# Performance work log

Measured on AMD Instinct MI355X. Metric: run time of the kernel, lower is better.

## Reference

```python
import jax, jax.numpy as jnp
import numpy as np

E, T, N = 120000, 800000, 12000
H, INT, BE, R, S, NB = 128, 64, 8, 6, 7, 2
SR = S * R  # 42 = num_spherical * num_radial
OE, OC = 256, 1
CUTOFF = 5.0
P_ENV = 6  # envelope_exponent + 1


def _glorot(k, shape):
    fan = shape[-2] + shape[-1]
    return jax.random.normal(k, shape, jnp.float32) * jnp.sqrt(2.0 / fan)


def setup_inputs() -> dict:
    key = jax.random.key(0)
    ki = iter(jax.random.split(key, 40))
    inp = {}
    inp["x"] = jax.random.normal(next(ki), (E, H), jnp.float32)
    # distances in (0.5, 4.9) so envelope 1/d term is well behaved
    inp["dist"] = 0.5 + 4.4 * jax.random.uniform(next(ki), (E,), jnp.float32)
    inp["freq"] = jnp.arange(1, R + 1, dtype=jnp.float32) * jnp.pi  # BesselBasisLayer init
    inp["sbf"] = jax.random.normal(next(ki), (T, SR), jnp.float32)
    inp["idx_kj"] = jax.random.randint(next(ki), (T,), 0, E)
    inp["idx_ji"] = jax.random.randint(next(ki), (T,), 0, E)
    inp["edge_i"] = jax.random.randint(next(ki), (E,), 0, N)
    inp["num_nodes"] = N
    inp["Wi_rbf1"] = _glorot(next(ki), (NB, R, BE))
    inp["Wi_rbf2"] = _glorot(next(ki), (NB, BE, H))
    inp["Wi_sbf1"] = _glorot(next(ki), (NB, SR, BE))
    inp["Wi_sbf2"] = _glorot(next(ki), (NB, BE, INT))
    inp["Wi_kj"] = _glorot(next(ki), (NB, H, H))
    inp["bi_kj"] = jnp.zeros((NB, H), jnp.float32)
    inp["Wi_ji"] = _glorot(next(ki), (NB, H, H))
    inp["bi_ji"] = jnp.zeros((NB, H), jnp.float32)
    inp["Wi_down"] = _glorot(next(ki), (NB, H, INT))
    inp["Wi_up"] = _glorot(next(ki), (NB, INT, H))
    inp["Wi_res"] = _glorot(next(ki), (NB, 3, 2, H, H))  # 1 before-skip + 2 after-skip residuals
    inp["bi_res"] = jnp.zeros((NB, 3, 2, H), jnp.float32)
    inp["Wi_lin"] = _glorot(next(ki), (NB, H, H))
    inp["bi_lin"] = jnp.zeros((NB, H), jnp.float32)
    inp["Wo_rbf"] = _glorot(next(ki), (NB + 1, R, H))
    inp["Wo_up"] = _glorot(next(ki), (NB + 1, H, OE))
    inp["bo_up"] = jnp.zeros((NB + 1, OE), jnp.float32)
    inp["Wo_lin"] = _glorot(next(ki), (NB + 1, 3, OE, OE))
    inp["bo_lin"] = jnp.zeros((NB + 1, 3, OE), jnp.float32)
    inp["Wo_out"] = _glorot(next(ki), (NB + 1, OE, OC))
    return inp


def reference(x, dist, freq, sbf,
              Wi_rbf1, Wi_rbf2, Wi_sbf1, Wi_sbf2, Wi_kj, bi_kj, Wi_ji, bi_ji,
              Wi_down, Wi_up, Wi_res, bi_res, Wi_lin, bi_lin,
              Wo_rbf, Wo_up, bo_up, Wo_lin, bo_lin, Wo_out,
              idx_kj, idx_ji, edge_i, num_nodes):
    act = jax.nn.silu  # swish
    num_edges = x.shape[0]

    # BesselBasisLayer with Envelope(p=6): a=-28, b=48, c=-21
    d = dist / CUTOFF                       # [E]
    d5 = d ** (P_ENV - 1)
    env = 1.0 / d - 28.0 * d5 + 48.0 * d5 * d - 21.0 * d5 * d * d
    rbf = env[:, None] * jnp.sin(freq[None, :] * d[:, None])  # [E, R]

    def output_block(b, xe):
        g = (rbf @ Wo_rbf[b]) * xe                                   # [E, H]
        nodes = jax.ops.segment_sum(g, edge_i, num_segments=num_nodes)  # [N, H]
        h = nodes @ Wo_up[b] + bo_up[b]
        for l in range(Wo_lin.shape[1]):
            h = act(h @ Wo_lin[b, l] + bo_lin[b, l])
        return h @ Wo_out[b]                                          # [N, OC]

    def residual(b, r, h):
        t = act(h @ Wi_res[b, r, 0] + bi_res[b, r, 0])
        return h + act(t @ Wi_res[b, r, 1] + bi_res[b, r, 1])

    def interaction(b, xe):
        x_ji = act(xe @ Wi_ji[b] + bi_ji[b])                          # [E, H]
        x_kj = act(xe @ Wi_kj[b] + bi_kj[b])                          # [E, H]
        rb = (rbf @ Wi_rbf1[b]) @ Wi_rbf2[b]                          # [E, H]
        x_kj = act((x_kj * rb) @ Wi_down[b])                          # [E, INT]
        sb = (sbf @ Wi_sbf1[b]) @ Wi_sbf2[b]                          # [T, INT]
        m = x_kj[idx_kj] * sb                                         # gather over triplets
        agg = jax.ops.segment_sum(m, idx_ji, num_segments=num_edges)  # scatter back to edges
        x_kj = act(agg @ Wi_up[b])                                    # [E, H]
        h = x_ji + x_kj
        h = residual(b, 0, h)                                         # before skip
        h = act(h @ Wi_lin[b] + bi_lin[b]) + xe                       # skip
        h = residual(b, 1, h)                                         # after skip
        h = residual(b, 2, h)
        return h

    P = output_block(0, x)
    xe = x
    for b in range(NB):
        xe = interaction(b, xe)
        P = P + output_block(b + 1, xe)
    return P  # [num_nodes, out_channels]
```

## Files before the change

### kernel.cpp

```cpp
#include <hip/hip_runtime.h>
#include <hip/hip_bf16.h>

namespace {
constexpr int E     = 120000;
constexpr int T     = 800000;
constexpr int NN    = 12000;
constexpr int H     = 128;
constexpr int INTD  = 64;
constexpr int BE    = 8;
constexpr int R     = 6;
constexpr int SR    = 42;
constexpr int OE    = 256;
constexpr float CUTOFF = 5.0f;
constexpr int PKB   = 163840;
constexpr int TAILO = 40960;
}

typedef __attribute__((ext_vector_type(8))) short bf16x8;
typedef __attribute__((ext_vector_type(4))) float f32x4;

__device__ __forceinline__ float silu_f(float x) { return x / (1.0f + __expf(-x)); }
__device__ __forceinline__ float4 silu4(float4 v) {
    return make_float4(silu_f(v.x), silu_f(v.y), silu_f(v.z), silu_f(v.w));
}

__device__ __forceinline__ unsigned fbits(float x) {
    union { float f; unsigned u; } v; v.f = x; return v.u;
}
__device__ __forceinline__ float fof(unsigned u) {
    union { float f; unsigned u; } v; v.u = u; return v.f;
}
__device__ __forceinline__ unsigned short bf16_rn(float x) {
    unsigned u = fbits(x);
    unsigned r = u + 0x7FFFu + ((u >> 16) & 1u);
    return (unsigned short)(r >> 16);
}
__device__ __forceinline__ float bf16_f(unsigned short h) { return fof(((unsigned)h) << 16); }

__device__ __forceinline__ void pack2(float x0, float x1, unsigned& h, unsigned& l) {
    const unsigned u0 = fbits(x0), u1 = fbits(x1);
    const unsigned t0 = u0 & 0xFFFF0000u, t1 = u1 & 0xFFFF0000u;
    h = (u0 >> 16) | t1;
    l = (fbits(x0 - fof(t0)) >> 16) | (fbits(x1 - fof(t1)) & 0xFFFF0000u);
}

__global__ void k_rbf(const float* __restrict__ dist, const float* __restrict__ freq,
                      float* __restrict__ rbf) {
    int e = blockIdx.x * blockDim.x + threadIdx.x;
    if (e >= E) return;
    float d  = dist[e] * (1.0f / CUTOFF);
    float d2 = d * d;
    float d5 = d2 * d2 * d;
    float env = 1.0f / d - 28.0f * d5 + 48.0f * d5 * d - 21.0f * d5 * d2;
    #pragma unroll
    for (int i = 0; i < R; ++i) rbf[e * R + i] = env * sinf(freq[i] * d);
}

__global__ void k_count(const int* __restrict__ idx, int n, int* __restrict__ cnt) {
    int i = blockIdx.x * 256 + threadIdx.x;
    if (i < n) atomicAdd(&cnt[idx[i]], 1);
}

__global__ __launch_bounds__(256) void k_red(const int* __restrict__ cnt, int n,
                                             int* __restrict__ bsum) {
    __shared__ int ws[4];
    const int tid = threadIdx.x;
    const int base = blockIdx.x * 2048 + tid * 8;
    int s = 0;
    #pragma unroll
    for (int k = 0; k < 8; ++k) { int i = base + k; s += (i < n) ? cnt[i] : 0; }
    #pragma unroll
    for (int off = 32; off; off >>= 1) s += __shfl_down(s, off);
    if ((tid & 63) == 0) ws[tid >> 6] = s;
    __syncthreads();
    if (tid == 0) bsum[blockIdx.x] = ws[0] + ws[1] + ws[2] + ws[3];
}

__global__ void k_scanb(int* __restrict__ b, int nb) {
    __shared__ int s[64];
    const int tid = threadIdx.x;
    if (tid < nb) s[tid] = b[tid];
    __syncthreads();
    if (tid == 0) {
        int run = 0;
        for (int i = 0; i < nb; ++i) { int c = s[i]; s[i] = run; run += c; }
    }
    __syncthreads();
    if (tid < nb) b[tid] = s[tid];
}

__global__ __launch_bounds__(256) void k_fill_rs(const int* __restrict__ cnt, int n,
                                                 const int* __restrict__ boff,
                                                 int* __restrict__ rs, int* __restrict__ cur) {
    __shared__ int ts[256];
    const int tid = threadIdx.x;
    const int base = blockIdx.x * 2048 + tid * 8;
    int v[8]; int s = 0;
    #pragma unroll
    for (int k = 0; k < 8; ++k) { int i = base + k; v[k] = (i < n) ? cnt[i] : 0; s += v[k]; }
    ts[tid] = s;
    __syncthreads();
    for (int off = 1; off < 256; off <<= 1) {
        int t = (tid >= off) ? ts[tid - off] : 0;
        __syncthreads();
        ts[tid] += t;
        __syncthreads();
    }
    int ex = boff[blockIdx.x] + ((tid == 0) ? 0 : ts[tid - 1]);
    #pragma unroll
    for (int k = 0; k < 8; ++k) {
        int i = base + k;
        if (i < n) {
            rs[i] = ex; cur[i] = ex; ex += v[k];
            if (i == n - 1) rs[n] = ex;
        }
    }
}

__global__ void k_fill(const int* __restrict__ idx, int n, int* __restrict__ cur,
                       int* __restrict__ perm) {
    int i = blockIdx.x * 256 + threadIdx.x;
    if (i < n) perm[atomicAdd(&cur[idx[i]], 1)] = i;
}

__global__ void k_fill_trip(const int* __restrict__ idx_ji, const int* __restrict__ idx_kj,
                            int n, int* __restrict__ cur,
                            int* __restrict__ kjs, int* __restrict__ rank) {
    int i = blockIdx.x * 256 + threadIdx.x;
    if (i < n) {
        int pos = atomicAdd(&cur[idx_ji[i]], 1);
        kjs[pos] = idx_kj[i];
        rank[i]  = pos;
    }
}

__global__ __launch_bounds__(256) void k_pack(
    const float* __restrict__ Wi_ji, const float* __restrict__ Wi_kj,
    const float* __restrict__ Wi_down,
    const float* __restrict__ Wi_up, const float* __restrict__ Wi_res,
    const float* __restrict__ Wi_lin,
    short* __restrict__ wh, short* __restrict__ wl)
{
    const int g = blockIdx.x * 256 + threadIdx.x;
    if (g >= 2 * PKB) return;
    const int b = g / PKB;
    const int off = g % PKB;
    const float* W;
    int rel, NT;
    if (off < 16384)      { W = Wi_ji   + (size_t)b * 16384; rel = off;          NT = 8; }
    else if (off < 32768) { W = Wi_kj   + (size_t)b * 16384; rel = off - 16384;  NT = 8; }
    else if (off < 40960) { W = Wi_down + (size_t)b * 8192;  rel = off - 32768;  NT = 4; }
    else if (off < 49152) { W = Wi_up   + (size_t)b * 8192;  rel = off - 40960;  NT = 8; }
    else {
        const int i = (off - 49152) / 16384;
        rel = (off - 49152) % 16384;
        NT = 8;
        if (i == 2) W = Wi_lin + (size_t)b * 16384;
        else {
            const int idx = (i < 2) ? i : i - 1;
            W = Wi_res + (size_t)((b * 3 + idx / 2) * 2 + (idx & 1)) * 16384;
        }
    }
    const int j = rel & 7, lane = (rel >> 3) & 63, q = rel >> 9;
    const int nt = q % NT, kt = q / NT;
    const int k = kt * 32 + (lane >> 4) * 8 + j;
    const int n = nt * 16 + (lane & 15);
    const float x = W[(size_t)k * (NT * 16) + n];
    const unsigned short h = bf16_rn(x);
    wh[g] = (short)h;
    wl[g] = (short)bf16_rn(x - bf16_f(h));
}

__global__ __launch_bounds__(256) void k_sbfproj2(
    const float* __restrict__ sbf, const float* __restrict__ W1a,
    const float* __restrict__ W1b, const int* __restrict__ rank,
    float* __restrict__ ta, float* __restrict__ tb)
{
    __shared__ float s_sbf[32 * SR];
    __shared__ float s_Wa[SR * BE];
    __shared__ float s_Wb[SR * BE];
    const int tid = threadIdx.x;
    const int t0  = blockIdx.x * 32;
    for (int i = tid; i < SR * BE; i += 256) { s_Wa[i] = W1a[i]; s_Wb[i] = W1b[i]; }
    const float* sb0 = sbf + (size_t)t0 * SR;
    for (int i = tid; i < 32 * SR; i += 256) s_sbf[i] = sb0[i];
    __syncthreads();
    const int tt = tid >> 3, j = tid & 7;
    float sa = 0.0f, sb = 0.0f;
    #pragma unroll
    for (int i = 0; i < SR; ++i) {
        const float v = s_sbf[tt * SR + i];
        sa = fmaf(v, s_Wa[i * BE + j], sa);
        sb = fmaf(v, s_Wb[i * BE + j], sb);
    }
    const size_t p = (size_t)rank[t0 + tt] * BE + j;
    ta[p] = sa;
    tb[p] = sb;
}

__global__ __launch_bounds__(256, 2) void k_front_mfma(
    const float* __restrict__ xe, const float* __restrict__ rbf,
    const short* __restrict__ wh, const short* __restrict__ wl,
    const float* __restrict__ bji, const float* __restrict__ bkj,
    const float* __restrict__ W1, const float* __restrict__ W2,
    float* __restrict__ xji, float* __restrict__ down)
{
    __shared__ short Ah[64 * 136];
    __shared__ short Al[64 * 136];
    __shared__ float s_tj[64 * 8];
    const int tid = threadIdx.x;
    const int r0  = blockIdx.x * 64;
    const int lane = tid & 63, wv = tid >> 6;
    const int lo4 = lane & 15, hi4 = lane >> 4;

    {
        const float4* XG = reinterpret_cast<const float4*>(xe);
        for (int i = tid; i < 64 * 32; i += 256) {
            const int row = i >> 5, c4 = i & 31;
            const float4 v = XG[(size_t)(r0 + row) * 32 + c4];
            unsigned h0, l0, h1, l1;
            pack2(v.x, v.y, h0, l0);
            pack2(v.z, v.w, h1, l1);
            *reinterpret_cast<uint2*>(&Ah[row * 136 + c4 * 4]) = make_uint2(h0, h1);
            *reinterpret_cast<uint2*>(&Al[row * 136 + c4 * 4]) = make_uint2(l0, l1);
        }
    }
    for (int i = tid; i < 64 * 8; i += 256) {
        const int row = i >> 3, j = i & 7;
        const float* rr_ = rbf + (size_t)(r0 + row) * R;
        float s = 0.0f;
        #pragma unroll
        for (int q = 0; q < R; ++q) s = fmaf(rr_[q], W1[q * BE + j], s);
        s_tj[i] = s;
    }
    __syncthreads();

    f32x4 acc[4][2], car[4][2];

    auto gemm = [&](const short* Wh, const short* Wl) {
        #pragma unroll
        for (int m = 0; m < 4; ++m)
            #pragma unroll
            for (int n = 0; n < 2; ++n) acc[m][n] = (f32x4)0.0f;
        for (int kt = 0; kt < 4; ++kt) {
            bf16x8 xh[4], xl[4], whf[2], wlf[2];
            #pragma unroll
            for (int m = 0; m < 4; ++m) {
                const int off = (m * 16 + lo4) * 136 + kt * 32 + hi4 * 8;
                xh[m] = *reinterpret_cast<const bf16x8*>(&Ah[off]);
                xl[m] = *reinterpret_cast<const bf16x8*>(&Al[off]);
            }
            #pragma unroll
            for (int n = 0; n < 2; ++n) {
                const size_t boff = ((size_t)((kt * 8 + wv * 2 + n) * 64) + lane) * 8;
                whf[n] = *reinterpret_cast<const bf16x8*>(&Wh[boff]);
                wlf[n] = *reinterpret_cast<const bf16x8*>(&Wl[boff]);
            }
            #pragma unroll
            for (int m = 0; m < 4; ++m)
                #pragma unroll
                for (int n = 0; n < 2; ++n) {
                    acc[m][n] = __builtin_amdgcn_mfma_f32_16x16x32_bf16(whf[n], xh[m], acc[m][n], 0, 0, 0);
                    acc[m][n] = __builtin_amdgcn_mfma_f32_16x16x32_bf16(wlf[n], xh[m], acc[m][n], 0, 0, 0);
                    acc[m][n] = __builtin_amdgcn_mfma_f32_16x16x32_bf16(whf[n], xl[m], acc[m][n], 0, 0, 0);
                }
        }
    };

    gemm(wh, wl);
    #pragma unroll
    for (int n = 0; n < 2; ++n) {
        const int feat0 = (wv * 2 + n) * 16 + hi4 * 4;
        const float4 bj = *reinterpret_cast<const float4*>(&bji[feat0]);
        #pragma unroll
        for (int m = 0; m < 4; ++m) {
            const int edge = r0 + m * 16 + lo4;
            float4 o = make_float4(silu_f(acc[m][n][0] + bj.x), silu_f(acc[m][n][1] + bj.y),
                                   silu_f(acc[m][n][2] + bj.z), silu_f(acc[m][n][3] + bj.w));
            *reinterpret_cast<float4*>(&xji[(size_t)edge * 128 + feat0]) = o;
        }
    }

    gemm(wh + 16384, wl + 16384);
    #pragma unroll
    for (int n = 0; n < 2; ++n) {
        const int feat0 = (wv * 2 + n) * 16 + hi4 * 4;
        const float4 bk = *reinterpret_cast<const float4*>(&bkj[feat0]);
        float4 w2v[8];
        #pragma unroll
        for (int j = 0; j < 8; ++j)
            w2v[j] = *reinterpret_cast<const float4*>(&W2[j * 128 + feat0]);
        #pragma unroll
        for (int m = 0; m < 4; ++m) {
            const int erow = m * 16 + lo4;
            const float4 t0 = *reinterpret_cast<const float4*>(&s_tj[erow * 8]);
            const float4 t1 = *reinterpret_cast<const float4*>(&s_tj[erow * 8 + 4]);
            float rb0 = 0, rb1 = 0, rb2 = 0, rb3 = 0;
            const float tj[8] = {t0.x, t0.y, t0.z, t0.w, t1.x, t1.y, t1.z, t1.w};
            #pragma unroll
            for (int j = 0; j < 8; ++j) {
                rb0 = fmaf(tj[j], w2v[j].x, rb0); rb1 = fmaf(tj[j], w2v[j].y, rb1);
                rb2 = fmaf(tj[j], w2v[j].z, rb2); rb3 = fmaf(tj[j], w2v[j].w, rb3);
            }
            car[m][n][0] = silu_f(acc[m][n][0] + bk.x) * rb0;
            car[m][n][1] = silu_f(acc[m][n][1] + bk.y) * rb1;
            car[m][n][2] = silu_f(acc[m][n][2] + bk.z) * rb2;
            car[m][n][3] = silu_f(acc[m][n][3] + bk.w) * rb3;
        }
    }
    __syncthreads();
    #pragma unroll
    for (int m = 0; m < 4; ++m) {
        const int edge = m * 16 + lo4;
        #pragma unroll
        for (int n = 0; n < 2; ++n) {
            const int feat0 = (wv * 2 + n) * 16 + hi4 * 4;
            unsigned h0, l0, h1, l1;
            pack2(car[m][n][0], car[m][n][1], h0, l0);
            pack2(car[m][n][2], car[m][n][3], h1, l1);
            *reinterpret_cast<uint2*>(&Ah[edge * 136 + feat0]) = make_uint2(h0, h1);
            *reinterpret_cast<uint2*>(&Al[edge * 136 + feat0]) = make_uint2(l0, l1);
        }
    }
    __syncthreads();

    {
        const short* Wh = wh + 32768;
        const short* Wl = wl + 32768;
        f32x4 a2[4];
        #pragma unroll
        for (int m = 0; m < 4; ++m) a2[m] = (f32x4)0.0f;
        for (int kt = 0; kt < 4; ++kt) {
            bf16x8 xh[4], xl[4], whf, wlf;
            #pragma unroll
            for (int m = 0; m < 4; ++m) {
                const int off = (m * 16 + lo4) * 136 + kt * 32 + hi4 * 8;
                xh[m] = *reinterpret_cast<const bf16x8*>(&Ah[off]);
                xl[m] = *reinterpret_cast<const bf16x8*>(&Al[off]);
            }
            const size_t boff = ((size_t)((kt * 4 + wv) * 64) + lane) * 8;
            whf = *reinterpret_cast<const bf16x8*>(&Wh[boff]);
            wlf = *reinterpret_cast<const bf16x8*>(&Wl[boff]);
            #pragma unroll
            for (int m = 0; m < 4; ++m) {
                a2[m] = __builtin_amdgcn_mfma_f32_16x16x32_bf16(whf, xh[m], a2[m], 0, 0, 0);
                a2[m] = __builtin_amdgcn_mfma_f32_16x16x32_bf16(wlf, xh[m], a2[m], 0, 0, 0);
                a2[m] = __builtin_amdgcn_mfma_f32_16x16x32_bf16(whf, xl[m], a2[m], 0, 0, 0);
            }
        }
        const int feat0 = wv * 16 + hi4 * 4;
        #pragma unroll
        for (int m = 0; m < 4; ++m) {
            const int edge = r0 + m * 16 + lo4;
            *reinterpret_cast<float4*>(&down[(size_t)edge * 64 + feat0]) =
                make_float4(silu_f(a2[m][0]), silu_f(a2[m][1]),
                            silu_f(a2[m][2]), silu_f(a2[m][3]));
        }
    }
}

__global__ __launch_bounds__(256) void k_agg(
    const int* __restrict__ rs, const int* __restrict__ kjs,
    const float* __restrict__ tmps, const float* __restrict__ down,
    const float* __restrict__ W2, float* __restrict__ agg)
{
    const int w = threadIdx.x >> 6, lane = threadIdx.x & 63;
    const int e = blockIdx.x * 4 + w;
    float w2[BE];
    #pragma unroll
    for (int j = 0; j < BE; ++j) w2[j] = W2[j * INTD + lane];

    const float4* tmps4 = reinterpret_cast<const float4*>(tmps);
    const int lo = rs[e], hi = rs[e + 1];
    float acc = 0.0f;
    int idx = lo;
    for (; idx + 1 < hi; idx += 2) {
        const int kja = kjs[idx], kjb = kjs[idx + 1];
        const float4 a0 = tmps4[2 * idx],     a1 = tmps4[2 * idx + 1];
        const float4 b0 = tmps4[2 * idx + 2], b1 = tmps4[2 * idx + 3];
        const float da = down[(size_t)kja * INTD + lane];
        const float db = down[(size_t)kjb * INTD + lane];
        float sa = a0.x * w2[0] + a0.y * w2[1] + a0.z * w2[2] + a0.w * w2[3]
                 + a1.x * w2[4] + a1.y * w2[5] + a1.z * w2[6] + a1.w * w2[7];
        float sb = b0.x * w2[0] + b0.y * w2[1] + b0.z * w2[2] + b0.w * w2[3]
                 + b1.x * w2[4] + b1.y * w2[5] + b1.z * w2[6] + b1.w * w2[7];
        acc = fmaf(da, sa, acc);
        acc = fmaf(db, sb, acc);
    }
    if (idx < hi) {
        const int kj = kjs[idx];
        const float4 a0 = tmps4[2 * idx], a1 = tmps4[2 * idx + 1];
        const float d = down[(size_t)kj * INTD + lane];
        float sa = a0.x * w2[0] + a0.y * w2[1] + a0.z * w2[2] + a0.w * w2[3]
                 + a1.x * w2[4] + a1.y * w2[5] + a1.z * w2[6] + a1.w * w2[7];
        acc = fmaf(d, sa, acc);
    }
    agg[(size_t)e * INTD + lane] = acc;
}

__global__ __launch_bounds__(256, 2) void k_tail_mfma(
    const float* __restrict__ agg, const float* __restrict__ xji,
    const float* __restrict__ xe,
    const short* __restrict__ wh, const short* __restrict__ wl,
    const float* __restrict__ br, const float* __restrict__ blin,
    float* __restrict__ out)
{
    __shared__ short Ah[64 * 136];
    __shared__ short Al[64 * 136];
    const int tid = threadIdx.x;
    const int r0  = blockIdx.x * 64;
    const int lane = tid & 63, wv = tid >> 6;
    const int lo4 = lane & 15, hi4 = lane >> 4;

    {
        const float4* AG = reinterpret_cast<const float4*>(agg);
        for (int i = tid; i < 64 * 16; i += 256) {
            const int row = i >> 4, c4 = i & 15;
            const float4 v = AG[(size_t)(r0 + row) * 16 + c4];
            unsigned h0, l0, h1, l1;
            pack2(v.x, v.y, h0, l0);
            pack2(v.z, v.w, h1, l1);
            *reinterpret_cast<uint2*>(&Ah[row * 136 + c4 * 4]) = make_uint2(h0, h1);
            *reinterpret_cast<uint2*>(&Al[row * 136 + c4 * 4]) = make_uint2(l0, l1);
        }
    }
    __syncthreads();

    f32x4 acc[4][2], car[4][2];

    auto gemm = [&](const short* Wh, const short* Wl, int nkt) {
        #pragma unroll
        for (int m = 0; m < 4; ++m)
            #pragma unroll
            for (int n = 0; n < 2; ++n) acc[m][n] = (f32x4)0.0f;
        for (int kt = 0; kt < nkt; ++kt) {
            bf16x8 xh[4], xl[4], whf[2], wlf[2];
            #pragma unroll
            for (int m = 0; m < 4; ++m) {
                const int off = (m * 16 + lo4) * 136 + kt * 32 + hi4 * 8;
                xh[m] = *reinterpret_cast<const bf16x8*>(&Ah[off]);
                xl[m] = *reinterpret_cast<const bf16x8*>(&Al[off]);
            }
            #pragma unroll
            for (int n = 0; n < 2; ++n) {
                const size_t boff = ((size_t)((kt * 8 + wv * 2 + n) * 64) + lane) * 8;
                whf[n] = *reinterpret_cast<const bf16x8*>(&Wh[boff]);
                wlf[n] = *reinterpret_cast<const bf16x8*>(&Wl[boff]);
            }
            #pragma unroll
            for (int m = 0; m < 4; ++m)
                #pragma unroll
                for (int n = 0; n < 2; ++n) {
                    acc[m][n] = __builtin_amdgcn_mfma_f32_16x16x32_bf16(whf[n], xh[m], acc[m][n], 0, 0, 0);
                    acc[m][n] = __builtin_amdgcn_mfma_f32_16x16x32_bf16(wlf[n], xh[m], acc[m][n], 0, 0, 0);
                    acc[m][n] = __builtin_amdgcn_mfma_f32_16x16x32_bf16(whf[n], xl[m], acc[m][n], 0, 0, 0);
                }
        }
    };

    auto wrA = [&](f32x4 v[4][2]) {
        __syncthreads();
        #pragma unroll
        for (int m = 0; m < 4; ++m) {
            const int edge = m * 16 + lo4;
            #pragma unroll
            for (int n = 0; n < 2; ++n) {
                const int feat0 = (wv * 2 + n) * 16 + hi4 * 4;
                unsigned h0, l0, h1, l1;
                pack2(v[m][n][0], v[m][n][1], h0, l0);
                pack2(v[m][n][2], v[m][n][3], h1, l1);
                *reinterpret_cast<uint2*>(&Ah[edge * 136 + feat0]) = make_uint2(h0, h1);
                *reinterpret_cast<uint2*>(&Al[edge * 136 + feat0]) = make_uint2(l0, l1);
            }
        }
        __syncthreads();
    };

    gemm(wh, wl, 2);
    #pragma unroll
    for (int n = 0; n < 2; ++n) {
        const int feat0 = (wv * 2 + n) * 16 + hi4 * 4;
        #pragma unroll
        for (int m = 0; m < 4; ++m) {
            const int edge = r0 + m * 16 + lo4;
            const float4 xv = *reinterpret_cast<const float4*>(&xji[(size_t)edge * 128 + feat0]);
            car[m][n][0] = silu_f(acc[m][n][0]) + xv.x;
            car[m][n][1] = silu_f(acc[m][n][1]) + xv.y;
            car[m][n][2] = silu_f(acc[m][n][2]) + xv.z;
            car[m][n][3] = silu_f(acc[m][n][3]) + xv.w;
        }
    }
    wrA(car);

    auto tphase = [&](const short* Wh, const short* Wl, const float* bias) {
        gemm(Wh, Wl, 4);
        #pragma unroll
        for (int n = 0; n < 2; ++n) {
            const int feat0 = (wv * 2 + n) * 16 + hi4 * 4;
            const float4 bv = *reinterpret_cast<const float4*>(&bias[feat0]);
            #pragma unroll
            for (int m = 0; m < 4; ++m) {
                acc[m][n][0] = silu_f(acc[m][n][0] + bv.x);
                acc[m][n][1] = silu_f(acc[m][n][1] + bv.y);
                acc[m][n][2] = silu_f(acc[m][n][2] + bv.z);
                acc[m][n][3] = silu_f(acc[m][n][3] + bv.w);
            }
        }
        wrA(acc);
    };
    auto cphase = [&](const short* Wh, const short* Wl, const float* bias) {
        gemm(Wh, Wl, 4);
        #pragma unroll
        for (int n = 0; n < 2; ++n) {
            const int feat0 = (wv * 2 + n) * 16 + hi4 * 4;
            const float4 bv = *reinterpret_cast<const float4*>(&bias[feat0]);
            #pragma unroll
            for (int m = 0; m < 4; ++m) {
                car[m][n][0] += silu_f(acc[m][n][0] + bv.x);
                car[m][n][1] += silu_f(acc[m][n][1] + bv.y);
                car[m][n][2] += silu_f(acc[m][n][2] + bv.z);
                car[m][n][3] += silu_f(acc[m][n][3] + bv.w);
            }
        }
        wrA(car);
    };

    tphase(wh + 8192,              wl + 8192,              br + 0 * 128);
    cphase(wh + 8192 + 16384,      wl + 8192 + 16384,      br + 1 * 128);

    gemm(wh + 8192 + 2 * 16384, wl + 8192 + 2 * 16384, 4);
    #pragma unroll
    for (int n = 0; n < 2; ++n) {
        const int feat0 = (wv * 2 + n) * 16 + hi4 * 4;
        const float4 bv = *reinterpret_cast<const float4*>(&blin[feat0]);
        #pragma unroll
        for (int m = 0; m < 4; ++m) {
            const int edge = r0 + m * 16 + lo4;
            const float4 xv = *reinterpret_cast<const float4*>(&xe[(size_t)edge * 128 + feat0]);
            car[m][n][0] = silu_f(acc[m][n][0] + bv.x) + xv.x;
            car[m][n][1] = silu_f(acc[m][n][1] + bv.y) + xv.y;
            car[m][n][2] = silu_f(acc[m][n][2] + bv.z) + xv.z;
            car[m][n][3] = silu_f(acc[m][n][3] + bv.w) + xv.w;
        }
    }
    wrA(car);

    tphase(wh + 8192 + 3 * 16384, wl + 8192 + 3 * 16384, br + 2 * 128);
    cphase(wh + 8192 + 4 * 16384, wl + 8192 + 4 * 16384, br + 3 * 128);
    tphase(wh + 8192 + 5 * 16384, wl + 8192 + 5 * 16384, br + 4 * 128);

    gemm(wh + 8192 + 6 * 16384, wl + 8192 + 6 * 16384, 4);
    #pragma unroll
    for (int n = 0; n < 2; ++n) {
        const int feat0 = (wv * 2 + n) * 16 + hi4 * 4;
        const float4 bv = *reinterpret_cast<const float4*>(&br[5 * 128 + feat0]);
        #pragma unroll
        for (int m = 0; m < 4; ++m) {
            const int edge = r0 + m * 16 + lo4;
            float4 o = make_float4(car[m][n][0] + silu_f(acc[m][n][0] + bv.x),
                                   car[m][n][1] + silu_f(acc[m][n][1] + bv.y),
                                   car[m][n][2] + silu_f(acc[m][n][2] + bv.z),
                                   car[m][n][3] + silu_f(acc[m][n][3] + bv.w));
            *reinterpret_cast<float4*>(&out[(size_t)edge * 128 + feat0]) = o;
        }
    }
}

__global__ __launch_bounds__(256) void k_nodes(
    const int* __restrict__ rs, const int* __restrict__ perm,
    const float* __restrict__ rbf, const float* __restrict__ Wrbf,
    const float* __restrict__ xe, float* __restrict__ nodes)
{
    const int tid = threadIdx.x;
    const int n = blockIdx.x * 2 + (tid >> 7);
    const int c = tid & (H - 1);
    float wr[R];
    #pragma unroll
    for (int i = 0; i < R; ++i) wr[i] = Wrbf[i * H + c];
    float acc = 0.0f;
    const int lo = rs[n], hi = rs[n + 1];
    for (int idx = lo; idx < hi; ++idx) {
        const int e = perm[idx];
        const float* rb = rbf + (size_t)e * R;
        float g = 0.0f;
        #pragma unroll
        for (int i = 0; i < R; ++i) g = fmaf(rb[i], wr[i], g);
        acc = fmaf(g, xe[(size_t)e * H + c], acc);
    }
    nodes[(size_t)n * H + c] = acc;
}

__global__ __launch_bounds__(256) void k_outchain(
    const float* __restrict__ nodes, const float* __restrict__ Wup,
    const float* __restrict__ bup, const float* __restrict__ Wlin,
    const float* __restrict__ blin, const float* __restrict__ Wout,
    float* __restrict__ P)
{
    __shared__ float nb[16 * 132];
    __shared__ float hb[16 * 260];
    __shared__ float tbuf[16 * 260];
    __shared__ float red[64 * 16];
    const int tid = threadIdx.x;
    const int n0  = blockIdx.x * 16;
    float4* nb4 = reinterpret_cast<float4*>(nb);
    float4* hb4 = reinterpret_cast<float4*>(hb);
    float4* tb4 = reinterpret_cast<float4*>(tbuf);
    const float4* NG = reinterpret_cast<const float4*>(nodes);

    for (int i = tid; i < 16 * 32; i += 256) {
        int row = i >> 5, kk = i & 31;
        nb4[row * 33 + kk] = NG[(size_t)(n0 + row) * 32 + kk];
    }
    __syncthreads();

    const int cg = tid & 63, rq = tid >> 6, rbase = rq * 4;
    float acc[4][4];
    auto acc_bias = [&](const float* bias) {
        const float4 bv = reinterpret_cast<const float4*>(bias)[cg];
        #pragma unroll
        for (int r = 0; r < 4; ++r) { acc[r][0]=bv.x; acc[r][1]=bv.y; acc[r][2]=bv.z; acc[r][3]=bv.w; }
    };
    auto mm = [&](const float4* A4, const float4* W4, int K4, int AS4) {
        for (int k4 = 0; k4 < K4; ++k4) {
            const float4 wv0 = W4[(k4*4+0)*64 + cg];
            const float4 wv1 = W4[(k4*4+1)*64 + cg];
            const float4 wv2 = W4[(k4*4+2)*64 + cg];
            const float4 wv3 = W4[(k4*4+3)*64 + cg];
            #pragma unroll
            for (int r = 0; r < 4; ++r) {
                const float4 a = A4[(rbase + r) * AS4 + k4];
                acc[r][0]=fmaf(a.x,wv0.x,acc[r][0]); acc[r][1]=fmaf(a.x,wv0.y,acc[r][1]);
                acc[r][2]=fmaf(a.x,wv0.z,acc[r][2]); acc[r][3]=fmaf(a.x,wv0.w,acc[r][3]);
                acc[r][0]=fmaf(a.y,wv1.x,acc[r][0]); acc[r][1]=fmaf(a.y,wv1.y,acc[r][1]);
                acc[r][2]=fmaf(a.y,wv1.z,acc[r][2]); acc[r][3]=fmaf(a.y,wv1.w,acc[r][3]);
                acc[r][0]=fmaf(a.z,wv2.x,acc[r][0]); acc[r][1]=fmaf(a.z,wv2.y,acc[r][1]);
                acc[r][2]=fmaf(a.z,wv2.z,acc[r][2]); acc[r][3]=fmaf(a.z,wv2.w,acc[r][3]);
                acc[r][0]=fmaf(a.w,wv3.x,acc[r][0]); acc[r][1]=fmaf(a.w,wv3.y,acc[r][1]);
                acc[r][2]=fmaf(a.w,wv3.z,acc[r][2]); acc[r][3]=fmaf(a.w,wv3.w,acc[r][3]);
            }
        }
    };

    acc_bias(bup);
    mm(nb4, reinterpret_cast<const float4*>(Wup), 32, 33);
    #pragma unroll
    for (int r = 0; r < 4; ++r) hb4[(rbase + r) * 65 + cg] = make_float4(acc[r][0],acc[r][1],acc[r][2],acc[r][3]);
    __syncthreads();

    acc_bias(blin + 0 * OE);
    mm(hb4, reinterpret_cast<const float4*>(Wlin + 0 * OE * OE), 64, 65);
    #pragma unroll
    for (int r = 0; r < 4; ++r) tb4[(rbase + r) * 65 + cg] = silu4(make_float4(acc[r][0],acc[r][1],acc[r][2],acc[r][3]));
    __syncthreads();

    acc_bias(blin + 1 * OE);
    mm(tb4, reinterpret_cast<const float4*>(Wlin + 1 * OE * OE), 64, 65);
    #pragma unroll
    for (int r = 0; r < 4; ++r) hb4[(rbase + r) * 65 + cg] = silu4(make_float4(acc[r][0],acc[r][1],acc[r][2],acc[r][3]));
    __syncthreads();

    acc_bias(blin + 2 * OE);
    mm(hb4, reinterpret_cast<const float4*>(Wlin + 2 * OE * OE), 64, 65);
    #pragma unroll
    for (int r = 0; r < 4; ++r) tb4[(rbase + r) * 65 + cg] = silu4(make_float4(acc[r][0],acc[r][1],acc[r][2],acc[r][3]));
    __syncthreads();

    {
        const float4 wo = reinterpret_cast<const float4*>(Wout)[cg];
        #pragma unroll
        for (int r = 0; r < 4; ++r) {
            const int row = rbase + r;
            const float4 hv = tb4[row * 65 + cg];
            red[cg * 16 + row] = hv.x * wo.x + hv.y * wo.y + hv.z * wo.z + hv.w * wo.w;
        }
    }
    __syncthreads();
    if (tid < 16) {
        float s = 0.0f;
        for (int c = 0; c < 64; ++c) s += red[c * 16 + tid];
        P[n0 + tid] += s;
    }
}

extern "C" void kernel_launch(void* const* d_in, const int* in_sizes, int n_in,
                              void* d_out, int out_size, void* d_ws, size_t ws_size,
                              hipStream_t stream)
{
    (void)in_sizes; (void)n_in; (void)out_size; (void)ws_size;

    const float* x       = (const float*)d_in[0];
    const float* dist    = (const float*)d_in[1];
    const float* freq    = (const float*)d_in[2];
    const float* sbf     = (const float*)d_in[3];
    const int*   idx_kj  = (const int*)d_in[4];
    const int*   idx_ji  = (const int*)d_in[5];
    const int*   edge_i  = (const int*)d_in[6];
    const float* Wi_rbf1 = (const float*)d_in[8];
    const float* Wi_rbf2 = (const float*)d_in[9];
    const float* Wi_sbf1 = (const float*)d_in[10];
    const float* Wi_sbf2 = (const float*)d_in[11];
    const float* Wi_kj   = (const float*)d_in[12];
    const float* bi_kj   = (const float*)d_in[13];
    const float* Wi_ji   = (const float*)d_in[14];
    const float* bi_ji   = (const float*)d_in[15];
    const float* Wi_down = (const float*)d_in[16];
    const float* Wi_up   = (const float*)d_in[17];
    const float* Wi_res  = (const float*)d_in[18];
    const float* bi_res  = (const float*)d_in[19];
    const float* Wi_lin  = (const float*)d_in[20];
    const float* bi_lin  = (const float*)d_in[21];
    const float* Wo_rbf  = (const float*)d_in[22];
    const float* Wo_up   = (const float*)d_in[23];
    const float* bo_up   = (const float*)d_in[24];
    const float* Wo_lin  = (const float*)d_in[25];
    const float* bo_lin  = (const float*)d_in[26];
    const float* Wo_out  = (const float*)d_in[27];
    float* P = (float*)d_out;

    float* w      = (float*)d_ws;
    float* rbf    = w;  w += (size_t)E * R;
    float* xeA    = w;  w += (size_t)E * H;
    float* xeB    = w;  w += (size_t)E * H;
    float* xji    = w;  w += (size_t)E * H;
    float* down   = w;  w += (size_t)E * INTD;
    float* agg    = w;  w += (size_t)E * INTD;
    float* tmp0   = w;  w += (size_t)T * BE;
    float* tmp1   = w;  w += (size_t)T * BE;
    float* nodes  = w;  w += (size_t)NN * H;
    int* ip       = (int*)w;
    int* trip_rs  = ip;  ip += E + 1;
    int* trip_cur = ip;  ip += E;
    int* rank_t   = ip;  ip += T;
    int* kjs      = ip;  ip += T;
    int* edge_rs  = ip;  ip += NN + 1;
    int* edge_cur = ip;  ip += NN;
    int* perm_e   = ip;  ip += E;
    int* bsumT    = ip;  ip += 64;
    int* bsumE    = ip;  ip += 64;
    short* wpk_hi = (short*)ip;
    short* wpk_lo = wpk_hi + 2 * PKB;

    hipMemsetAsync(trip_cur, 0, (size_t)E * sizeof(int), stream);
    hipMemsetAsync(edge_cur, 0, (size_t)NN * sizeof(int), stream);
    k_count<<<(T + 255) / 256, 256, 0, stream>>>(idx_ji, T, trip_cur);
    k_count<<<(E + 255) / 256, 256, 0, stream>>>(edge_i, E, edge_cur);
    const int nbT = (E + 2047) / 2048, nbE = (NN + 2047) / 2048;
    k_red<<<nbT, 256, 0, stream>>>(trip_cur, E, bsumT);
    k_scanb<<<1, 64, 0, stream>>>(bsumT, nbT);
    k_fill_rs<<<nbT, 256, 0, stream>>>(trip_cur, E, bsumT, trip_rs, trip_cur);
    k_red<<<nbE, 256, 0, stream>>>(edge_cur, NN, bsumE);
    k_scanb<<<1, 64, 0, stream>>>(bsumE, nbE);
    k_fill_rs<<<nbE, 256, 0, stream>>>(edge_cur, NN, bsumE, edge_rs, edge_cur);
    k_fill_trip<<<(T + 255) / 256, 256, 0, stream>>>(idx_ji, idx_kj, T, trip_cur, kjs, rank_t);
    k_fill<<<(E + 255) / 256, 256, 0, stream>>>(edge_i, E, edge_cur, perm_e);

    hipMemsetAsync(d_out, 0, (size_t)NN * sizeof(float), stream);
    k_rbf<<<(E + 255) / 256, 256, 0, stream>>>(dist, freq, rbf);
    k_pack<<<(2 * PKB + 255) / 256, 256, 0, stream>>>(Wi_ji, Wi_kj, Wi_down,
                                                      Wi_up, Wi_res, Wi_lin,
                                                      wpk_hi, wpk_lo);
    k_sbfproj2<<<T / 32, 256, 0, stream>>>(sbf, Wi_sbf1, Wi_sbf1 + (size_t)SR * BE,
                                           rank_t, tmp0, tmp1);

    auto out_block = [&](int b, const float* xe) {
        k_nodes<<<NN / 2, 256, 0, stream>>>(edge_rs, perm_e, rbf,
                                            Wo_rbf + (size_t)b * R * H, xe, nodes);
        k_outchain<<<NN / 16, 256, 0, stream>>>(nodes,
                                                Wo_up + (size_t)b * H * OE,
                                                bo_up + (size_t)b * OE,
                                                Wo_lin + (size_t)b * 3 * OE * OE,
                                                bo_lin + (size_t)b * 3 * OE,
                                                Wo_out + (size_t)b * OE, P);
    };

    const int gE64 = E / 64;
    auto interact = [&](int b, const float* xe, const float* tmp, float* out) {
        k_front_mfma<<<gE64, 256, 0, stream>>>(xe, rbf,
                                               wpk_hi + (size_t)b * PKB,
                                               wpk_lo + (size_t)b * PKB,
                                               bi_ji + (size_t)b * H,
                                               bi_kj + (size_t)b * H,
                                               Wi_rbf1 + (size_t)b * R * BE,
                                               Wi_rbf2 + (size_t)b * BE * H,
                                               xji, down);
        k_agg<<<E / 4, 256, 0, stream>>>(trip_rs, kjs, tmp, down,
                                         Wi_sbf2 + (size_t)b * BE * INTD, agg);
        k_tail_mfma<<<gE64, 256, 0, stream>>>(agg, xji, xe,
                                              wpk_hi + (size_t)b * PKB + TAILO,
                                              wpk_lo + (size_t)b * PKB + TAILO,
                                              bi_res + (size_t)b * 3 * 2 * H,
                                              bi_lin + (size_t)b * H, out);
    };

    out_block(0, x);
    interact(0, x, tmp0, xeB);
    out_block(1, xeB);
    interact(1, xeB, tmp1, xeA);
    out_block(2, xeA);
}
```

Baseline: 1.347 ms.

## Port output-block MLP chain to split-bf16 MFMA and raise launch bounds

Replaces the FP32 FMA output chain (up-projection plus three 256x256 layers per node tile) with an MFMA kernel. It uses hi/lo bf16 splitting for near-FP32 accuracy, with the Wo_up and Wo_lin weights prepacked by a new pack kernel. Node tiles grow from 16 to 32 rows, and intermediates stay in shared memory as bf16 pairs. The launch-bounds occupancy hint also rises from 2 to 4 on the front and tail MFMA kernels, which may force register spills. The extra pack kernel and workspace add some setup cost.

Result: slower. 1.398 ms (+3.7%).

```diff
diff --git a/kernel.cpp b/kernel.cpp
--- a/kernel.cpp
+++ b/kernel.cpp
@@ -14,15 +14,13 @@
 constexpr float CUTOFF = 5.0f;
 constexpr int PKB   = 163840;
 constexpr int TAILO = 40960;
+constexpr int OPKB  = 229376;
 }
 
 typedef __attribute__((ext_vector_type(8))) short bf16x8;
 typedef __attribute__((ext_vector_type(4))) float f32x4;
 
 __device__ __forceinline__ float silu_f(float x) { return x / (1.0f + __expf(-x)); }
-__device__ __forceinline__ float4 silu4(float4 v) {
-    return make_float4(silu_f(v.x), silu_f(v.y), silu_f(v.z), silu_f(v.w));
-}
 
 __device__ __forceinline__ unsigned fbits(float x) {
     union { float f; unsigned u; } v; v.f = x; return v.u;
@@ -171,6 +169,32 @@
     wl[g] = (short)bf16_rn(x - bf16_f(h));
 }
 
+__global__ __launch_bounds__(256) void k_packo(
+    const float* __restrict__ Wo_up, const float* __restrict__ Wo_lin,
+    short* __restrict__ wh, short* __restrict__ wl)
+{
+    const int g = blockIdx.x * 256 + threadIdx.x;
+    if (g >= 3 * OPKB) return;
+    const int b = g / OPKB;
+    const int off = g % OPKB;
+    const float* W;
+    int rel;
+    if (off < 32768) { W = Wo_up + (size_t)b * 32768; rel = off; }
+    else {
+        const int l = (off - 32768) / 65536;
+        rel = (off - 32768) % 65536;
+        W = Wo_lin + (size_t)(b * 3 + l) * 65536;
+    }
+    const int j = rel & 7, lane = (rel >> 3) & 63, q = rel >> 9;
+    const int nt = q % 16, kt = q / 16;
+    const int k = kt * 32 + (lane >> 4) * 8 + j;
+    const int n = nt * 16 + (lane & 15);
+    const float x = W[(size_t)k * 256 + n];
+    const unsigned short h = bf16_rn(x);
+    wh[g] = (short)h;
+    wl[g] = (short)bf16_rn(x - bf16_f(h));
+}
+
 __global__ __launch_bounds__(256) void k_sbfproj2(
     const float* __restrict__ sbf, const float* __restrict__ W1a,
     const float* __restrict__ W1b, const int* __restrict__ rank,
@@ -198,7 +222,7 @@
     tb[p] = sb;
 }
 
-__global__ __launch_bounds__(256, 2) void k_front_mfma(
+__global__ __launch_bounds__(256, 4) void k_front_mfma(
     const float* __restrict__ xe, const float* __restrict__ rbf,
     const short* __restrict__ wh, const short* __restrict__ wl,
     const float* __restrict__ bji, const float* __restrict__ bkj,
@@ -398,7 +422,7 @@
     agg[(size_t)e * INTD + lane] = acc;
 }
 
-__global__ __launch_bounds__(256, 2) void k_tail_mfma(
+__global__ __launch_bounds__(256, 4) void k_tail_mfma(
     const float* __restrict__ agg, const float* __restrict__ xji,
     const float* __restrict__ xe,
     const short* __restrict__ wh, const short* __restrict__ wl,
@@ -590,94 +614,118 @@
     nodes[(size_t)n * H + c] = acc;
 }
 
-__global__ __launch_bounds__(256) void k_outchain(
-    const float* __restrict__ nodes, const float* __restrict__ Wup,
-    const float* __restrict__ bup, const float* __restrict__ Wlin,
+__global__ __launch_bounds__(256, 4) void k_outchain_mfma(
+    const float* __restrict__ nodes, const short* __restrict__ wh,
+    const short* __restrict__ wl, const float* __restrict__ bup,
     const float* __restrict__ blin, const float* __restrict__ Wout,
     float* __restrict__ P)
 {
-    __shared__ float nb[16 * 132];
-    __shared__ float hb[16 * 260];
-    __shared__ float tbuf[16 * 260];
-    __shared__ float red[64 * 16];
+    __shared__ short Ah[32 * 264];
+    __shared__ short Al[32 * 264];
+    __shared__ float red[32 * 17];
     const int tid = threadIdx.x;
-    const int n0  = blockIdx.x * 16;
-    float4* nb4 = reinterpret_cast<float4*>(nb);
-    float4* hb4 = reinterpret_cast<float4*>(hb);
-    float4* tb4 = reinterpret_cast<float4*>(tbuf);
-    const float4* NG = reinterpret_cast<const float4*>(nodes);
-
-    for (int i = tid; i < 16 * 32; i += 256) {
-        int row = i >> 5, kk = i & 31;
-        nb4[row * 33 + kk] = NG[(size_t)(n0 + row) * 32 + kk];
-    }
-    __syncthreads();
-
-    const int cg = tid & 63, rq = tid >> 6, rbase = rq * 4;
-    float acc[4][4];
-    auto acc_bias = [&](const float* bias) {
-        const float4 bv = reinterpret_cast<const float4*>(bias)[cg];
-        #pragma unroll
-        for (int r = 0; r < 4; ++r) { acc[r][0]=bv.x; acc[r][1]=bv.y; acc[r][2]=bv.z; acc[r][3]=bv.w; }
+    const int n0  = blockIdx.x * 32;
+    const int lane = tid & 63, wv = tid >> 6;
+    const int lo4 = lane & 15, hi4 = lane >> 4;
+
+    {
+        const float4* NG = reinterpret_cast<const float4*>(nodes);
+        for (int i = tid; i < 32 * 32; i += 256) {
+            const int row = i >> 5, c4 = i & 31;
+            const float4 v = NG[(size_t)(n0 + row) * 32 + c4];
+            unsigned h0, l0, h1, l1;
+            pack2(v.x, v.y, h0, l0);
+            pack2(v.z, v.w, h1, l1);
+            *reinterpret_cast<uint2*>(&Ah[row * 264 + c4 * 4]) = make_uint2(h0, h1);
+            *reinterpret_cast<uint2*>(&Al[row * 264 + c4 * 4]) = make_uint2(l0, l1);
+        }
+    }
+    __syncthreads();
+
+    f32x4 acc[2][4];
+
+    auto gemm = [&](const short* Wh, const short* Wl, int nkt) {
+        #pragma unroll
+        for (int m = 0; m < 2; ++m)
+            #pragma unroll
+            for (int n = 0; n < 4; ++n) acc[m][n] = (f32x4)0.0f;
+        for (int kt = 0; kt < nkt; ++kt) {
+            bf16x8 xh[2], xl[2], whf[4], wlf[4];
+            #pragma unroll
+            for (int m = 0; m < 2; ++m) {
+                const int off = (m * 16 + lo4) * 264 + kt * 32 + hi4 * 8;
+                xh[m] = *reinterpret_cast<const bf16x8*>(&Ah[off]);
+                xl[m] = *reinterpret_cast<const bf16x8*>(&Al[off]);
+            }
+            #pragma unroll
+            for (int n = 0; n < 4; ++n) {
+                const size_t boff = ((size_t)((kt * 16 + wv * 4 + n) * 64) + lane) * 8;
+                whf[n] = *reinterpret_cast<const bf16x8*>(&Wh[boff]);
+                wlf[n] = *reinterpret_cast<const bf16x8*>(&Wl[boff]);
+            }
+            #pragma unroll
+            for (int m = 0; m < 2; ++m)
+                #pragma unroll
+                for (int n = 0; n < 4; ++n) {
+                    acc[m][n] = __builtin_amdgcn_mfma_f32_16x16x32_bf16(whf[n], xh[m], acc[m][n], 0, 0, 0);
+                    acc[m][n] = __builtin_amdgcn_mfma_f32_16x16x32_bf16(wlf[n], xh[m], acc[m][n], 0, 0, 0);
+                    acc[m][n] = __builtin_amdgcn_mfma_f32_16x16x32_bf16(whf[n], xl[m], acc[m][n], 0, 0, 0);
+                }
+        }
     };
-    auto mm = [&](const float4* A4, const float4* W4, int K4, int AS4) {
-        for (int k4 = 0; k4 < K4; ++k4) {
-            const float4 wv0 = W4[(k4*4+0)*64 + cg];
-            const float4 wv1 = W4[(k4*4+1)*64 + cg];
-            const float4 wv2 = W4[(k4*4+2)*64 + cg];
-            const float4 wv3 = W4[(k4*4+3)*64 + cg];
-            #pragma unroll
-            for (int r = 0; r < 4; ++r) {
-                const float4 a = A4[(rbase + r) * AS4 + k4];
-                acc[r][0]=fmaf(a.x,wv0.x,acc[r][0]); acc[r][1]=fmaf(a.x,wv0.y,acc[r][1]);
-                acc[r][2]=fmaf(a.x,wv0.z,acc[r][2]); acc[r][3]=fmaf(a.x,wv0.w,acc[r][3]);
-                acc[r][0]=fmaf(a.y,wv1.x,acc[r][0]); acc[r][1]=fmaf(a.y,wv1.y,acc[r][1]);
-                acc[r][2]=fmaf(a.y,wv1.z,acc[r][2]); acc[r][3]=fmaf(a.y,wv1.w,acc[r][3]);
-                acc[r][0]=fmaf(a.z,wv2.x,acc[r][0]); acc[r][1]=fmaf(a.z,wv2.y,acc[r][1]);
-                acc[r][2]=fmaf(a.z,wv2.z,acc[r][2]); acc[r][3]=fmaf(a.z,wv2.w,acc[r][3]);
-                acc[r][0]=fmaf(a.w,wv3.x,acc[r][0]); acc[r][1]=fmaf(a.w,wv3.y,acc[r][1]);
-                acc[r][2]=fmaf(a.w,wv3.z,acc[r][2]); acc[r][3]=fmaf(a.w,wv3.w,acc[r][3]);
-            }
-        }
+
+    auto wrA = [&](bool dosilu, const float* bias) {
+        __syncthreads();
+        #pragma unroll
+        for (int m = 0; m < 2; ++m) {
+            const int node = m * 16 + lo4;
+            #pragma unroll
+            for (int n = 0; n < 4; ++n) {
+                const int feat0 = (wv * 4 + n) * 16 + hi4 * 4;
+                const float4 bv = *reinterpret_cast<const float4*>(&bias[feat0]);
+                float v0 = acc[m][n][0] + bv.x, v1 = acc[m][n][1] + bv.y;
+                float v2 = acc[m][n][2] + bv.z, v3 = acc[m][n][3] + bv.w;
+                if (dosilu) { v0 = silu_f(v0); v1 = silu_f(v1); v2 = silu_f(v2); v3 = silu_f(v3); }
+                unsigned h0, l0, h1, l1;
+                pack2(v0, v1, h0, l0);
+                pack2(v2, v3, h1, l1);
+                *reinterpret_cast<uint2*>(&Ah[node * 264 + feat0]) = make_uint2(h0, h1);
+                *reinterpret_cast<uint2*>(&Al[node * 264 + feat0]) = make_uint2(l0, l1);
+            }
+        }
+        __syncthreads();
     };
 
-    acc_bias(bup);
-    mm(nb4, reinterpret_cast<const float4*>(Wup), 32, 33);
-    #pragma unroll
-    for (int r = 0; r < 4; ++r) hb4[(rbase + r) * 65 + cg] = make_float4(acc[r][0],acc[r][1],acc[r][2],acc[r][3]);
-    __syncthreads();
-
-    acc_bias(blin + 0 * OE);
-    mm(hb4, reinterpret_cast<const float4*>(Wlin + 0 * OE * OE), 64, 65);
-    #pragma unroll
-    for (int r = 0; r < 4; ++r) tb4[(rbase + r) * 65 + cg] = silu4(make_float4(acc[r][0],acc[r][1],acc[r][2],acc[r][3]));
-    __syncthreads();
-
-    acc_bias(blin + 1 * OE);
-    mm(tb4, reinterpret_cast<const float4*>(Wlin + 1 * OE * OE), 64, 65);
-    #pragma unroll
-    for (int r = 0; r < 4; ++r) hb4[(rbase + r) * 65 + cg] = silu4(make_float4(acc[r][0],acc[r][1],acc[r][2],acc[r][3]));
-    __syncthreads();
-
-    acc_bias(blin + 2 * OE);
-    mm(hb4, reinterpret_cast<const float4*>(Wlin + 2 * OE * OE), 64, 65);
-    #pragma unroll
-    for (int r = 0; r < 4; ++r) tb4[(rbase + r) * 65 + cg] = silu4(make_float4(acc[r][0],acc[r][1],acc[r][2],acc[r][3]));
-    __syncthreads();
-
-    {
-        const float4 wo = reinterpret_cast<const float4*>(Wout)[cg];
-        #pragma unroll
-        for (int r = 0; r < 4; ++r) {
-            const int row = rbase + r;
-            const float4 hv = tb4[row * 65 + cg];
-            red[cg * 16 + row] = hv.x * wo.x + hv.y * wo.y + hv.z * wo.z + hv.w * wo.w;
-        }
-    }
-    __syncthreads();
-    if (tid < 16) {
+    gemm(wh, wl, 4);
+    wrA(false, bup);
+    gemm(wh + 32768, wl + 32768, 8);
+    wrA(true, blin + 0 * OE);
+    gemm(wh + 32768 + 65536, wl + 32768 + 65536, 8);
+    wrA(true, blin + 1 * OE);
+    gemm(wh + 32768 + 2 * 65536, wl + 32768 + 2 * 65536, 8);
+
+    float part[2] = {0.0f, 0.0f};
+    #pragma unroll
+    for (int n = 0; n < 4; ++n) {
+        const int feat0 = (wv * 4 + n) * 16 + hi4 * 4;
+        const float4 bv = *reinterpret_cast<const float4*>(&blin[2 * OE + feat0]);
+        const float4 wo = *reinterpret_cast<const float4*>(&Wout[feat0]);
+        #pragma unroll
+        for (int m = 0; m < 2; ++m) {
+            part[m] += silu_f(acc[m][n][0] + bv.x) * wo.x
+                     + silu_f(acc[m][n][1] + bv.y) * wo.y
+                     + silu_f(acc[m][n][2] + bv.z) * wo.z
+                     + silu_f(acc[m][n][3] + bv.w) * wo.w;
+        }
+    }
+    #pragma unroll
+    for (int m = 0; m < 2; ++m)
+        red[(m * 16 + lo4) * 17 + wv * 4 + hi4] = part[m];
+    __syncthreads();
+    if (tid < 32) {
         float s = 0.0f;
-        for (int c = 0; c < 64; ++c) s += red[c * 16 + tid];
+        #pragma unroll
+        for (int c = 0; c < 16; ++c) s += red[tid * 17 + c];
         P[n0 + tid] += s;
     }
 }
@@ -739,6 +787,8 @@
     int* bsumE    = ip;  ip += 64;
     short* wpk_hi = (short*)ip;
     short* wpk_lo = wpk_hi + 2 * PKB;
+    short* wo_hi  = wpk_lo + 2 * PKB;
+    short* wo_lo  = wo_hi + 3 * OPKB;
 
     hipMemsetAsync(trip_cur, 0, (size_t)E * sizeof(int), stream);
     hipMemsetAsync(edge_cur, 0, (size_t)NN * sizeof(int), stream);
@@ -759,18 +809,19 @@
     k_pack<<<(2 * PKB + 255) / 256, 256, 0, stream>>>(Wi_ji, Wi_kj, Wi_down,
                                                       Wi_up, Wi_res, Wi_lin,
                                                       wpk_hi, wpk_lo);
+    k_packo<<<(3 * OPKB + 255) / 256, 256, 0, stream>>>(Wo_up, Wo_lin, wo_hi, wo_lo);
     k_sbfproj2<<<T / 32, 256, 0, stream>>>(sbf, Wi_sbf1, Wi_sbf1 + (size_t)SR * BE,
                                            rank_t, tmp0, tmp1);
 
     auto out_block = [&](int b, const float* xe) {
         k_nodes<<<NN / 2, 256, 0, stream>>>(edge_rs, perm_e, rbf,
                                             Wo_rbf + (size_t)b * R * H, xe, nodes);
-        k_outchain<<<NN / 16, 256, 0, stream>>>(nodes,
-                                                Wo_up + (size_t)b * H * OE,
-                                                bo_up + (size_t)b * OE,
-                                                Wo_lin + (size_t)b * 3 * OE * OE,
-                                                bo_lin + (size_t)b * 3 * OE,
-                                                Wo_out + (size_t)b * OE, P);
+        k_outchain_mfma<<<NN / 32, 256, 0, stream>>>(nodes,
+                                                     wo_hi + (size_t)b * OPKB,
+                                                     wo_lo + (size_t)b * OPKB,
+                                                     bo_up + (size_t)b * OE,
+                                                     bo_lin + (size_t)b * 3 * OE,
+                                                     Wo_out + (size_t)b * OE, P);
     };
 
     const int gE64 = E / 64;
```
